# Kernel tuning notes

Measured on AMD Instinct MI355X. Metric: run time of the kernel, lower is better.

The kernel has to match this reference:

```python
import jax, jax.numpy as jnp
import numpy as np

B, G, CIN, COUT = 1024, 64, 512, 512  # G = s**(num_layers-1) = 2**6


def setup_inputs() -> dict:
    key = jax.random.key(0)
    kx, kw = jax.random.split(key)
    x = jax.random.normal(kx, (B, G, CIN), dtype=jnp.float32)
    weight = jax.random.normal(kw, (G, CIN, COUT), dtype=jnp.float32)
    return {"x": x, "weight": weight}


def reference(x, weight):
    # Original: (x[:,:,:,None] * W[None]).sum(2) / sqrt(Cin), then sum over groups.
    # Fused equivalent: grouped contraction over (g, c) -> [B, Cout].
    scale = 1.0 / jnp.sqrt(jnp.asarray(x.shape[2], dtype=x.dtype))
    out = jnp.einsum("bgc,gco->bo", x, weight) * scale
    return out
```

## Files before the change

### kernel.cpp

```cpp
#include <hip/hip_runtime.h>
#include <hip/hip_bf16.h>

typedef __bf16 bf16x8 __attribute__((ext_vector_type(8)));
typedef __bf16 bf16x4 __attribute__((ext_vector_type(4)));
typedef float  f32x4  __attribute__((ext_vector_type(4)));

#define B_SZ    1024
#define COUT_SZ 512
#define K_SZ    32768
#define TM 128
#define TN 128
#define BK 32

__device__ __forceinline__ void async_copy16(const void* g, void* l) {
  __builtin_amdgcn_global_load_lds(
      (const __attribute__((address_space(1))) unsigned int*)g,
      (__attribute__((address_space(3))) unsigned int*)l, 16, 0, 0);
}

#define XCVT_BLOCKS 2048
__global__ __launch_bounds__(256) void xcvt_kernel(
    const float* __restrict__ x, __bf16* __restrict__ xb) {
  const size_t stride = (size_t)XCVT_BLOCKS * 256 * 8;
  size_t i = ((size_t)blockIdx.x * 256 + threadIdx.x) * 8;
#pragma unroll
  for (int it = 0; it < 4; ++it) {
    f32x4 a0 = *(const f32x4*)(x + i);
    f32x4 c0 = *(const f32x4*)(x + i + 4);
    f32x4 a1 = *(const f32x4*)(x + i + stride);
    f32x4 c1 = *(const f32x4*)(x + i + stride + 4);
    bf16x8 o0, o1;
#pragma unroll
    for (int e = 0; e < 4; ++e) {
      o0[e] = (__bf16)a0[e]; o0[e + 4] = (__bf16)c0[e];
      o1[e] = (__bf16)a1[e]; o1[e + 4] = (__bf16)c1[e];
    }
    *(bf16x8*)(xb + i) = o0;
    *(bf16x8*)(xb + i + stride) = o1;
    i += 2 * stride;
  }
}

__global__ __launch_bounds__(256) void wtrans_kernel(
    const float* __restrict__ w, __bf16* __restrict__ wt) {
  __shared__ float t[64 * 65];
  const int kb = (blockIdx.x & 511) * 64;
  const int ob = (blockIdx.x >> 9) * 64;
  const int tid = threadIdx.x;
  {
    const int o4 = (tid & 15) * 4;
    const int kr = tid >> 4;
    const float* src = w + (size_t)(kb + kr) * COUT_SZ + ob + o4;
#pragma unroll
    for (int i = 0; i < 4; ++i) {
      f32x4 v = *(const f32x4*)(src + (size_t)(16 * i) * COUT_SZ);
      *(f32x4*)&t[(kr + 16 * i) * 65 + o4] = v;
    }
  }
  __syncthreads();
  {
    const int k4 = (tid & 15) * 4;
    const int orow = tid >> 4;
#pragma unroll
    for (int j = 0; j < 4; ++j) {
      const int o = orow + 16 * j;
      bf16x4 p;
#pragma unroll
      for (int e = 0; e < 4; ++e) p[e] = (__bf16)t[(k4 + e) * 65 + o];
      *(bf16x4*)(wt + (size_t)(ob + o) * K_SZ + kb + k4) = p;
    }
  }
}

__global__ __launch_bounds__(256, 4)
void gemm_kernel(const __bf16* __restrict__ xb, const __bf16* __restrict__ wt,
                 float* __restrict__ dst, int kchunk, int S) {
  __shared__ __bf16 As[TM * BK];
  __shared__ __bf16 Bs[TN * BK];

  const int lin = blockIdx.x;
  const int z = lin % S;
  const int t = lin / S;
  const int m0 = (t & 7) * TM;
  const int n0 = (t >> 3) * TN;
  const int tid  = threadIdx.x;
  const int w    = tid >> 6;
  const int lane = tid & 63;
  const int kbase = z * kchunk;

  const int sRow = lane >> 2;
  const int sCh  = (lane & 3) ^ (sRow & 3);
  const __bf16* ag0 = xb + (size_t)(m0 + w * 32 + sRow) * K_SZ + kbase + sCh * 8;
  const __bf16* ag1 = xb + (size_t)(m0 + w * 32 + 16 + sRow) * K_SZ + kbase + sCh * 8;
  const __bf16* bg0 = wt + (size_t)(n0 + w * 32 + sRow) * K_SZ + kbase + sCh * 8;
  const __bf16* bg1 = wt + (size_t)(n0 + w * 32 + 16 + sRow) * K_SZ + kbase + sCh * 8;
  __bf16* aL0 = &As[(w * 32) * BK];
  __bf16* aL1 = &As[(w * 32 + 16) * BK];
  __bf16* bL0 = &Bs[(w * 32) * BK];
  __bf16* bL1 = &Bs[(w * 32 + 16) * BK];

  const int lm = lane & 15;
  const int q  = lane >> 4;
  const int wm = (w & 1) * 64;
  const int wn = (w >> 1) * 64;
  const int pc = q ^ (lm & 3);

  f32x4 acc[4][4];
#pragma unroll
  for (int i = 0; i < 4; ++i)
#pragma unroll
    for (int j = 0; j < 4; ++j)
      acc[i][j] = (f32x4){0.f, 0.f, 0.f, 0.f};

  const int niter = kchunk / BK;
  for (int it = 0; it < niter; ++it) {
    async_copy16(ag0, aL0);
    async_copy16(ag1, aL1);
    async_copy16(bg0, bL0);
    async_copy16(bg1, bL1);
    ag0 += BK; ag1 += BK; bg0 += BK; bg1 += BK;
    __syncthreads();

    bf16x8 af[4], bfr[4];
#pragma unroll
    for (int i = 0; i < 4; ++i)
      af[i] = *(const bf16x8*)&As[(wm + i * 16 + lm) * BK + pc * 8];
#pragma unroll
    for (int j = 0; j < 4; ++j)
      bfr[j] = *(const bf16x8*)&Bs[(wn + j * 16 + lm) * BK + pc * 8];

#pragma unroll
    for (int i = 0; i < 4; ++i)
#pragma unroll
      for (int j = 0; j < 4; ++j)
        acc[i][j] = __builtin_amdgcn_mfma_f32_16x16x32_bf16(af[i], bfr[j], acc[i][j], 0, 0, 0);

    __syncthreads();
  }

  float* outp = dst + (size_t)z * (B_SZ * COUT_SZ)
              + (size_t)(m0 + wm + q * 4) * COUT_SZ + (n0 + wn + lm);
#pragma unroll
  for (int i = 0; i < 4; ++i) {
#pragma unroll
    for (int r = 0; r < 4; ++r) {
      float* o2 = outp + (size_t)(i * 16 + r) * COUT_SZ;
#pragma unroll
      for (int j = 0; j < 4; ++j)
        o2[j * 16] = acc[i][j][r];
    }
  }
}

__global__ __launch_bounds__(256) void reduce_kernel(
    const float* __restrict__ p, float* __restrict__ out, int S, float scale) {
  const int i = (blockIdx.x * 256 + threadIdx.x) * 4;
  f32x4 s0 = (f32x4){0.f, 0.f, 0.f, 0.f};
  f32x4 s1 = (f32x4){0.f, 0.f, 0.f, 0.f};
  int zz = 0;
  for (; zz + 1 < S; zz += 2) {
    s0 = s0 + *(const f32x4*)(p + (size_t)zz * (B_SZ * COUT_SZ) + i);
    s1 = s1 + *(const f32x4*)(p + (size_t)(zz + 1) * (B_SZ * COUT_SZ) + i);
  }
  for (; zz < S; ++zz)
    s0 = s0 + *(const f32x4*)(p + (size_t)zz * (B_SZ * COUT_SZ) + i);
  s0 = (s0 + s1) * scale;
  *(f32x4*)(out + i) = s0;
}

extern "C" void kernel_launch(void* const* d_in, const int* in_sizes, int n_in,
                              void* d_out, int out_size, void* d_ws, size_t ws_size,
                              hipStream_t stream) {
  const float* x = (const float*)d_in[0];
  const float* w = (const float*)d_in[1];
  float* out = (float*)d_out;

  const size_t wtB    = (size_t)COUT_SZ * K_SZ * sizeof(__bf16);
  const size_t xbB    = (size_t)B_SZ * K_SZ * sizeof(__bf16);
  const size_t sliceB = (size_t)B_SZ * COUT_SZ * sizeof(float);

  __bf16* wt = (__bf16*)d_ws;
  __bf16* xb = (__bf16*)((char*)d_ws + wtB);
  float* partials = (float*)((char*)d_ws + wtB + xbB);

  int S = 32;
  while (S > 1 && wtB + xbB + (size_t)S * sliceB > ws_size) S >>= 1;
  if (wtB + xbB + sliceB > ws_size) { partials = out; S = 1; }

  const float scale = 0.04419417382415922f;

  hipLaunchKernelGGL(xcvt_kernel, dim3(XCVT_BLOCKS), dim3(256), 0, stream, x, xb);
  hipLaunchKernelGGL(wtrans_kernel, dim3((K_SZ / 64) * (COUT_SZ / 64)), dim3(256),
                     0, stream, w, wt);
  hipLaunchKernelGGL(gemm_kernel, dim3(32 * S), dim3(256), 0, stream,
                     xb, wt, partials, K_SZ / S, S);
  hipLaunchKernelGGL(reduce_kernel, dim3(B_SZ * COUT_SZ / 1024), dim3(256), 0,
                     stream, partials, out, S, scale);
}
```

Baseline: 322.6 us.

## Fuse x fp32-to-bf16 conversion into GEMM loads and store bf16 partials

Removes the separate x conversion kernel and its bf16 workspace copy. The GEMM now loads fp32 x directly, converts it in registers and writes it into a padded LDS tile. Split-K partials are stored as bf16 instead of fp32, which halves the partial write and reduce traffic. The trade-off is synchronous global loads of A in the GEMM in place of async LDS copies, twice the bytes read for A across the 8 N-tiles, and lower precision in the partial sums.

```diff
diff --git a/kernel.cpp b/kernel.cpp
--- a/kernel.cpp
+++ b/kernel.cpp
@@ -11,34 +11,12 @@
 #define TM 128
 #define TN 128
 #define BK 32
+#define APITCH 36
 
 __device__ __forceinline__ void async_copy16(const void* g, void* l) {
   __builtin_amdgcn_global_load_lds(
       (const __attribute__((address_space(1))) unsigned int*)g,
       (__attribute__((address_space(3))) unsigned int*)l, 16, 0, 0);
-}
-
-#define XCVT_BLOCKS 2048
-__global__ __launch_bounds__(256) void xcvt_kernel(
-    const float* __restrict__ x, __bf16* __restrict__ xb) {
-  const size_t stride = (size_t)XCVT_BLOCKS * 256 * 8;
-  size_t i = ((size_t)blockIdx.x * 256 + threadIdx.x) * 8;
-#pragma unroll
-  for (int it = 0; it < 4; ++it) {
-    f32x4 a0 = *(const f32x4*)(x + i);
-    f32x4 c0 = *(const f32x4*)(x + i + 4);
-    f32x4 a1 = *(const f32x4*)(x + i + stride);
-    f32x4 c1 = *(const f32x4*)(x + i + stride + 4);
-    bf16x8 o0, o1;
-#pragma unroll
-    for (int e = 0; e < 4; ++e) {
-      o0[e] = (__bf16)a0[e]; o0[e + 4] = (__bf16)c0[e];
-      o1[e] = (__bf16)a1[e]; o1[e + 4] = (__bf16)c1[e];
-    }
-    *(bf16x8*)(xb + i) = o0;
-    *(bf16x8*)(xb + i + stride) = o1;
-    i += 2 * stride;
-  }
 }
 
 __global__ __launch_bounds__(256) void wtrans_kernel(
@@ -73,9 +51,9 @@
 }
 
 __global__ __launch_bounds__(256, 4)
-void gemm_kernel(const __bf16* __restrict__ xb, const __bf16* __restrict__ wt,
-                 float* __restrict__ dst, int kchunk, int S) {
-  __shared__ __bf16 As[TM * BK];
+void gemm_kernel(const float* __restrict__ x, const __bf16* __restrict__ wt,
+                 __bf16* __restrict__ dst, int kchunk, int S) {
+  __shared__ __bf16 As[TM * APITCH];
   __shared__ __bf16 Bs[TN * BK];
 
   const int lin = blockIdx.x;
@@ -88,14 +66,15 @@
   const int lane = tid & 63;
   const int kbase = z * kchunk;
 
+  const int ar = tid >> 1;
+  const int ah = tid & 1;
+  const float* ag = x + (size_t)(m0 + ar) * K_SZ + kbase + ah * 16;
+  __bf16* aw = &As[ar * APITCH + ah * 16];
+
   const int sRow = lane >> 2;
   const int sCh  = (lane & 3) ^ (sRow & 3);
-  const __bf16* ag0 = xb + (size_t)(m0 + w * 32 + sRow) * K_SZ + kbase + sCh * 8;
-  const __bf16* ag1 = xb + (size_t)(m0 + w * 32 + 16 + sRow) * K_SZ + kbase + sCh * 8;
   const __bf16* bg0 = wt + (size_t)(n0 + w * 32 + sRow) * K_SZ + kbase + sCh * 8;
   const __bf16* bg1 = wt + (size_t)(n0 + w * 32 + 16 + sRow) * K_SZ + kbase + sCh * 8;
-  __bf16* aL0 = &As[(w * 32) * BK];
-  __bf16* aL1 = &As[(w * 32 + 16) * BK];
   __bf16* bL0 = &Bs[(w * 32) * BK];
   __bf16* bL1 = &Bs[(w * 32 + 16) * BK];
 
@@ -114,17 +93,39 @@
 
   const int niter = kchunk / BK;
   for (int it = 0; it < niter; ++it) {
-    async_copy16(ag0, aL0);
-    async_copy16(ag1, aL1);
     async_copy16(bg0, bL0);
     async_copy16(bg1, bL1);
-    ag0 += BK; ag1 += BK; bg0 += BK; bg1 += BK;
+    bg0 += BK; bg1 += BK;
+    {
+      f32x4 p0 = *(const f32x4*)(ag);
+      f32x4 p1 = *(const f32x4*)(ag + 4);
+      f32x4 p2 = *(const f32x4*)(ag + 8);
+      f32x4 p3 = *(const f32x4*)(ag + 12);
+      ag += BK;
+      bf16x4 c0, c1, c2, c3;
+#pragma unroll
+      for (int e = 0; e < 4; ++e) {
+        c0[e] = (__bf16)p0[e]; c1[e] = (__bf16)p1[e];
+        c2[e] = (__bf16)p2[e]; c3[e] = (__bf16)p3[e];
+      }
+      *(bf16x4*)(aw)      = c0;
+      *(bf16x4*)(aw + 4)  = c1;
+      *(bf16x4*)(aw + 8)  = c2;
+      *(bf16x4*)(aw + 12) = c3;
+    }
     __syncthreads();
 
     bf16x8 af[4], bfr[4];
 #pragma unroll
-    for (int i = 0; i < 4; ++i)
-      af[i] = *(const bf16x8*)&As[(wm + i * 16 + lm) * BK + pc * 8];
+    for (int i = 0; i < 4; ++i) {
+      const __bf16* arow = &As[(wm + i * 16 + lm) * APITCH + q * 8];
+      bf16x4 lo = *(const bf16x4*)arow;
+      bf16x4 hi = *(const bf16x4*)(arow + 4);
+      bf16x8 a;
+#pragma unroll
+      for (int e = 0; e < 4; ++e) { a[e] = lo[e]; a[e + 4] = hi[e]; }
+      af[i] = a;
+    }
 #pragma unroll
     for (int j = 0; j < 4; ++j)
       bfr[j] = *(const bf16x8*)&Bs[(wn + j * 16 + lm) * BK + pc * 8];
@@ -138,34 +139,36 @@
     __syncthreads();
   }
 
-  float* outp = dst + (size_t)z * (B_SZ * COUT_SZ)
-              + (size_t)(m0 + wm + q * 4) * COUT_SZ + (n0 + wn + lm);
+  __bf16* outp = dst + (size_t)z * (B_SZ * COUT_SZ)
+               + (size_t)(m0 + wm + q * 4) * COUT_SZ + (n0 + wn + lm);
 #pragma unroll
   for (int i = 0; i < 4; ++i) {
 #pragma unroll
     for (int r = 0; r < 4; ++r) {
-      float* o2 = outp + (size_t)(i * 16 + r) * COUT_SZ;
+      __bf16* o2 = outp + (size_t)(i * 16 + r) * COUT_SZ;
 #pragma unroll
       for (int j = 0; j < 4; ++j)
-        o2[j * 16] = acc[i][j][r];
+        o2[j * 16] = (__bf16)acc[i][j][r];
     }
   }
 }
 
 __global__ __launch_bounds__(256) void reduce_kernel(
-    const float* __restrict__ p, float* __restrict__ out, int S, float scale) {
-  const int i = (blockIdx.x * 256 + threadIdx.x) * 4;
-  f32x4 s0 = (f32x4){0.f, 0.f, 0.f, 0.f};
-  f32x4 s1 = (f32x4){0.f, 0.f, 0.f, 0.f};
-  int zz = 0;
-  for (; zz + 1 < S; zz += 2) {
-    s0 = s0 + *(const f32x4*)(p + (size_t)zz * (B_SZ * COUT_SZ) + i);
-    s1 = s1 + *(const f32x4*)(p + (size_t)(zz + 1) * (B_SZ * COUT_SZ) + i);
+    const __bf16* __restrict__ p, float* __restrict__ out, int S, float scale) {
+  const size_t i = ((size_t)blockIdx.x * 256 + threadIdx.x) * 8;
+  float s[8];
+#pragma unroll
+  for (int e = 0; e < 8; ++e) s[e] = 0.f;
+  for (int zz = 0; zz < S; ++zz) {
+    bf16x8 v = *(const bf16x8*)(p + (size_t)zz * (B_SZ * COUT_SZ) + i);
+#pragma unroll
+    for (int e = 0; e < 8; ++e) s[e] += (float)v[e];
   }
-  for (; zz < S; ++zz)
-    s0 = s0 + *(const f32x4*)(p + (size_t)zz * (B_SZ * COUT_SZ) + i);
-  s0 = (s0 + s1) * scale;
-  *(f32x4*)(out + i) = s0;
+  f32x4 o0, o1;
+#pragma unroll
+  for (int e = 0; e < 4; ++e) { o0[e] = s[e] * scale; o1[e] = s[e + 4] * scale; }
+  *(f32x4*)(out + i) = o0;
+  *(f32x4*)(out + i + 4) = o1;
 }
 
 extern "C" void kernel_launch(void* const* d_in, const int* in_sizes, int n_in,
@@ -176,24 +179,20 @@
   float* out = (float*)d_out;
 
   const size_t wtB    = (size_t)COUT_SZ * K_SZ * sizeof(__bf16);
-  const size_t xbB    = (size_t)B_SZ * K_SZ * sizeof(__bf16);
-  const size_t sliceB = (size_t)B_SZ * COUT_SZ * sizeof(float);
+  const size_t sliceB = (size_t)B_SZ * COUT_SZ * sizeof(__bf16);
 
   __bf16* wt = (__bf16*)d_ws;
-  __bf16* xb = (__bf16*)((char*)d_ws + wtB);
-  float* partials = (float*)((char*)d_ws + wtB + xbB);
+  __bf16* partials = (__bf16*)((char*)d_ws + wtB);
 
   int S = 32;
-  while (S > 1 && wtB + xbB + (size_t)S * sliceB > ws_size) S >>= 1;
-  if (wtB + xbB + sliceB > ws_size) { partials = out; S = 1; }
+  while (S > 1 && wtB + (size_t)S * sliceB > ws_size) S >>= 1;
 
   const float scale = 0.04419417382415922f;
 
-  hipLaunchKernelGGL(xcvt_kernel, dim3(XCVT_BLOCKS), dim3(256), 0, stream, x, xb);
   hipLaunchKernelGGL(wtrans_kernel, dim3((K_SZ / 64) * (COUT_SZ / 64)), dim3(256),
                      0, stream, w, wt);
   hipLaunchKernelGGL(gemm_kernel, dim3(32 * S), dim3(256), 0, stream,
-                     xb, wt, partials, K_SZ / S, S);
-  hipLaunchKernelGGL(reduce_kernel, dim3(B_SZ * COUT_SZ / 1024), dim3(256), 0,
-                     stream, partials, out, S, scale);
+                     x, wt, partials, K_SZ / S, S);
+  hipLaunchKernelGGL(reduce_kernel, dim3(B_SZ * COUT_SZ / (256 * 8)), dim3(256),
+                     0, stream, partials, out, S, scale);
 }
```

New measurement: 297.4 us. 7.8% less time.

## Double-buffer GEMM LDS tiles and store split-K partials in bf16

Applied to the files above, without the earlier changes.

The GEMM main loop now uses two LDS buffers, issuing async global-to-LDS loads for the next K tile while computing on the current one, with one barrier per iteration instead of two. Split-K partial sums are written as bf16 instead of fp32, and the reduce kernel reads 8 bf16 values per thread. Together these aim to hide load latency and halve partial-sum memory traffic. The bf16 partials add rounding error in the accumulation, and the S=1 fallback that wrote directly to the output was removed.

```diff
diff --git a/kernel.cpp b/kernel.cpp
--- a/kernel.cpp
+++ b/kernel.cpp
@@ -74,9 +74,9 @@
 
 __global__ __launch_bounds__(256, 4)
 void gemm_kernel(const __bf16* __restrict__ xb, const __bf16* __restrict__ wt,
-                 float* __restrict__ dst, int kchunk, int S) {
-  __shared__ __bf16 As[TM * BK];
-  __shared__ __bf16 Bs[TN * BK];
+                 __bf16* __restrict__ dst, int kchunk, int S) {
+  __shared__ __bf16 As[2][TM * BK];
+  __shared__ __bf16 Bs[2][TN * BK];
 
   const int lin = blockIdx.x;
   const int z = lin % S;
@@ -94,10 +94,8 @@
   const __bf16* ag1 = xb + (size_t)(m0 + w * 32 + 16 + sRow) * K_SZ + kbase + sCh * 8;
   const __bf16* bg0 = wt + (size_t)(n0 + w * 32 + sRow) * K_SZ + kbase + sCh * 8;
   const __bf16* bg1 = wt + (size_t)(n0 + w * 32 + 16 + sRow) * K_SZ + kbase + sCh * 8;
-  __bf16* aL0 = &As[(w * 32) * BK];
-  __bf16* aL1 = &As[(w * 32 + 16) * BK];
-  __bf16* bL0 = &Bs[(w * 32) * BK];
-  __bf16* bL1 = &Bs[(w * 32 + 16) * BK];
+  const int aOff0 = (w * 32) * BK;
+  const int aOff1 = (w * 32 + 16) * BK;
 
   const int lm = lane & 15;
   const int q  = lane >> 4;
@@ -112,60 +110,70 @@
     for (int j = 0; j < 4; ++j)
       acc[i][j] = (f32x4){0.f, 0.f, 0.f, 0.f};
 
+  async_copy16(ag0, &As[0][aOff0]);
+  async_copy16(ag1, &As[0][aOff1]);
+  async_copy16(bg0, &Bs[0][aOff0]);
+  async_copy16(bg1, &Bs[0][aOff1]);
+  ag0 += BK; ag1 += BK; bg0 += BK; bg1 += BK;
+
   const int niter = kchunk / BK;
   for (int it = 0; it < niter; ++it) {
-    async_copy16(ag0, aL0);
-    async_copy16(ag1, aL1);
-    async_copy16(bg0, bL0);
-    async_copy16(bg1, bL1);
-    ag0 += BK; ag1 += BK; bg0 += BK; bg1 += BK;
     __syncthreads();
+    const int p = it & 1;
+    if (it + 1 < niter) {
+      const int np = p ^ 1;
+      async_copy16(ag0, &As[np][aOff0]);
+      async_copy16(ag1, &As[np][aOff1]);
+      async_copy16(bg0, &Bs[np][aOff0]);
+      async_copy16(bg1, &Bs[np][aOff1]);
+      ag0 += BK; ag1 += BK; bg0 += BK; bg1 += BK;
+    }
 
     bf16x8 af[4], bfr[4];
 #pragma unroll
     for (int i = 0; i < 4; ++i)
-      af[i] = *(const bf16x8*)&As[(wm + i * 16 + lm) * BK + pc * 8];
+      af[i] = *(const bf16x8*)&As[p][(wm + i * 16 + lm) * BK + pc * 8];
 #pragma unroll
     for (int j = 0; j < 4; ++j)
-      bfr[j] = *(const bf16x8*)&Bs[(wn + j * 16 + lm) * BK + pc * 8];
+      bfr[j] = *(const bf16x8*)&Bs[p][(wn + j * 16 + lm) * BK + pc * 8];
 
 #pragma unroll
     for (int i = 0; i < 4; ++i)
 #pragma unroll
       for (int j = 0; j < 4; ++j)
         acc[i][j] = __builtin_amdgcn_mfma_f32_16x16x32_bf16(af[i], bfr[j], acc[i][j], 0, 0, 0);
-
-    __syncthreads();
-  }
-
-  float* outp = dst + (size_t)z * (B_SZ * COUT_SZ)
-              + (size_t)(m0 + wm + q * 4) * COUT_SZ + (n0 + wn + lm);
+  }
+
+  __bf16* outp = dst + (size_t)z * (B_SZ * COUT_SZ)
+               + (size_t)(m0 + wm + q * 4) * COUT_SZ + (n0 + wn + lm);
 #pragma unroll
   for (int i = 0; i < 4; ++i) {
 #pragma unroll
     for (int r = 0; r < 4; ++r) {
-      float* o2 = outp + (size_t)(i * 16 + r) * COUT_SZ;
+      __bf16* o2 = outp + (size_t)(i * 16 + r) * COUT_SZ;
 #pragma unroll
       for (int j = 0; j < 4; ++j)
-        o2[j * 16] = acc[i][j][r];
+        o2[j * 16] = (__bf16)acc[i][j][r];
     }
   }
 }
 
 __global__ __launch_bounds__(256) void reduce_kernel(
-    const float* __restrict__ p, float* __restrict__ out, int S, float scale) {
-  const int i = (blockIdx.x * 256 + threadIdx.x) * 4;
-  f32x4 s0 = (f32x4){0.f, 0.f, 0.f, 0.f};
-  f32x4 s1 = (f32x4){0.f, 0.f, 0.f, 0.f};
-  int zz = 0;
-  for (; zz + 1 < S; zz += 2) {
-    s0 = s0 + *(const f32x4*)(p + (size_t)zz * (B_SZ * COUT_SZ) + i);
-    s1 = s1 + *(const f32x4*)(p + (size_t)(zz + 1) * (B_SZ * COUT_SZ) + i);
-  }
-  for (; zz < S; ++zz)
-    s0 = s0 + *(const f32x4*)(p + (size_t)zz * (B_SZ * COUT_SZ) + i);
-  s0 = (s0 + s1) * scale;
-  *(f32x4*)(out + i) = s0;
+    const __bf16* __restrict__ p, float* __restrict__ out, int S, float scale) {
+  const size_t i = ((size_t)blockIdx.x * 256 + threadIdx.x) * 8;
+  float s[8];
+#pragma unroll
+  for (int e = 0; e < 8; ++e) s[e] = 0.f;
+  for (int zz = 0; zz < S; ++zz) {
+    bf16x8 v = *(const bf16x8*)(p + (size_t)zz * (B_SZ * COUT_SZ) + i);
+#pragma unroll
+    for (int e = 0; e < 8; ++e) s[e] += (float)v[e];
+  }
+  f32x4 o0, o1;
+#pragma unroll
+  for (int e = 0; e < 4; ++e) { o0[e] = s[e] * scale; o1[e] = s[e + 4] * scale; }
+  *(f32x4*)(out + i) = o0;
+  *(f32x4*)(out + i + 4) = o1;
 }
 
 extern "C" void kernel_launch(void* const* d_in, const int* in_sizes, int n_in,
@@ -177,15 +185,14 @@
 
   const size_t wtB    = (size_t)COUT_SZ * K_SZ * sizeof(__bf16);
   const size_t xbB    = (size_t)B_SZ * K_SZ * sizeof(__bf16);
-  const size_t sliceB = (size_t)B_SZ * COUT_SZ * sizeof(float);
+  const size_t sliceB = (size_t)B_SZ * COUT_SZ * sizeof(__bf16);
 
   __bf16* wt = (__bf16*)d_ws;
   __bf16* xb = (__bf16*)((char*)d_ws + wtB);
-  float* partials = (float*)((char*)d_ws + wtB + xbB);
+  __bf16* partials = (__bf16*)((char*)d_ws + wtB + xbB);
 
   int S = 32;
   while (S > 1 && wtB + xbB + (size_t)S * sliceB > ws_size) S >>= 1;
-  if (wtB + xbB + sliceB > ws_size) { partials = out; S = 1; }
 
   const float scale = 0.04419417382415922f;
 
@@ -194,6 +201,6 @@
                      0, stream, w, wt);
   hipLaunchKernelGGL(gemm_kernel, dim3(32 * S), dim3(256), 0, stream,
                      xb, wt, partials, K_SZ / S, S);
-  hipLaunchKernelGGL(reduce_kernel, dim3(B_SZ * COUT_SZ / 1024), dim3(256), 0,
-                     stream, partials, out, S, scale);
-}
+  hipLaunchKernelGGL(reduce_kernel, dim3(B_SZ * COUT_SZ / (256 * 8)), dim3(256),
+                     0, stream, partials, out, S, scale);
+}
```

Result: faster. 314.9 us (-2.4%).
